# Performance work log

Measured on AMD Instinct MI355X. Metric: run time of the kernel, lower is better.

The kernel has to match this reference:

```python
import jax, jax.numpy as jnp
import numpy as np
from jax import lax

N = 8192

def _conv(x, w, b):
    # x: NCHW, w: OIHW, valid conv stride 1
    y = lax.conv_general_dilated(x, w, (1, 1), 'VALID',
                                 dimension_numbers=('NCHW', 'OIHW', 'NCHW'))
    return y + b[None, :, None, None]

def _maxpool2(x):
    return lax.reduce_window(x, -jnp.inf, lax.max, (1, 1, 2, 2), (1, 1, 2, 2), 'VALID')

def setup_inputs() -> dict:
    key = jax.random.key(0)
    ks = jax.random.split(key, 13)
    def rn(k, shape, scale):
        return jax.random.normal(k, shape, dtype=jnp.float32) * scale
    inp = {}
    inp['x'] = jax.random.normal(ks[0], (N, 3, 32, 32), dtype=jnp.float32)
    inp['W1'] = rn(ks[1], (6, 3, 5, 5), 0.1)
    inp['b1'] = rn(ks[2], (6,), 0.1)
    inp['W2'] = rn(ks[3], (16, 6, 5, 5), 0.08)
    inp['b2'] = rn(ks[4], (16,), 0.1)
    inp['Wf1'] = rn(ks[5], (120, 400), 0.05)
    inp['bf1'] = rn(ks[6], (120,), 0.05)
    inp['Wf2'] = rn(ks[7], (84, 120), 0.09)
    inp['bf2'] = rn(ks[8], (84,), 0.09)
    inp['Wg'] = rn(ks[9], (10, 84), 0.1)    # GATConv fc weight (no bias)
    inp['attn_l'] = rn(ks[10], (10,), 0.3)  # a_l (src)
    inp['attn_r'] = rn(ks[11], (10,), 0.3)  # a_r (dst)
    inp['bg'] = rn(ks[12], (10,), 0.1)      # GATConv output bias
    return inp

def reference(x, W1, b1, W2, b2, Wf1, bf1, Wf2, bf2, Wg, attn_l, attn_r, bg):
    # CNN feature extractor (LeNet style)
    h = _maxpool2(jax.nn.relu(_conv(x, W1, b1)))   # [N,6,14,14]
    h = _maxpool2(jax.nn.relu(_conv(h, W2, b2)))   # [N,16,5,5]
    h = h.reshape(-1, 16 * 5 * 5)                  # [N,400]
    h = jax.nn.relu(h @ Wf1.T + bf1)               # [N,120]
    h = jax.nn.relu(h @ Wf2.T + bf2)               # [N,84]
    # Single-head GAT over fully-connected graph (incl. self-loops):
    # equivalent dense formulation of DGL GATConv(84,10,1)
    z = h @ Wg.T                                    # [N,10]
    el = z @ attn_l                                 # src scores [N]
    er = z @ attn_r                                 # dst scores [N]
    # e[i,j]: edge src=j -> dst=i
    e = jax.nn.leaky_relu(er[:, None] + el[None, :], negative_slope=0.2)  # [N,N]
    alpha = jax.nn.softmax(e, axis=1)               # softmax over incoming edges
    out = alpha @ z + bg                            # [N,10]
    return out
```

## Files before the change

kernel.cpp:

```cpp
#include <hip/hip_runtime.h>
#include <hip/hip_bf16.h>

typedef _Float16 half8 __attribute__((ext_vector_type(8)));
typedef __attribute__((aligned(8))) half8 half8_a8;
typedef float floatx4 __attribute__((ext_vector_type(4)));

#define LOG2E 1.44269504088896340736f

__device__ __forceinline__ float pool4_dpp(float v) {
  int s1 = __builtin_amdgcn_update_dpp(0, __float_as_int(v), 0xB1, 0xF, 0xF, true);
  float v1 = fmaxf(v, __int_as_float(s1));
  int s2 = __builtin_amdgcn_update_dpp(0, __float_as_int(v1), 0x4E, 0xF, 0xF, true);
  return fmaxf(v1, __int_as_float(s2));
}

__global__ __launch_bounds__(256) void k_prep(const float* __restrict__ Wf1,
    const float* __restrict__ Wf2, const float* __restrict__ Wg,
    const float* __restrict__ W1, const float* __restrict__ W2,
    _Float16* __restrict__ w1f, _Float16* __restrict__ w2f,
    _Float16* __restrict__ wgf, _Float16* __restrict__ B1,
    _Float16* __restrict__ B2M) {
  const int i = blockIdx.x * 256 + threadIdx.x;
  if (i < 53248) {
    const int n = i / 416, k = i - n * 416;
    w1f[i] = (_Float16)((n < 120 && k < 400) ? Wf1[n * 400 + k] : 0.f);
  } else if (i < 65536) {
    const int j = i - 53248;
    const int n = j >> 7, k = j & 127;
    w2f[j] = (_Float16)((n < 84 && k < 120) ? Wf2[n * 120 + k] : 0.f);
  } else if (i < 67072) {
    const int g = i - 65536;
    const int n = g / 96, k = g - n * 96;
    wgf[g] = (_Float16)((n < 10 && k < 84) ? Wg[n * 84 + k] : 0.f);
  } else if (i < 73216) {
    const int g = i - 67072;
    const int n = g / 192, k = g - n * 192;
    const int co = n >> 2, cy = (n >> 1) & 1, cx = n & 1;
    const int pidx = k >> 3, j = k & 7;
    const int r = pidx >> 2, ci = pidx & 3;
    float v = 0.f;
    if (co < 6 && ci < 3) {
      const int ky = r - cy, kx = j - cx;
      if (ky >= 0 && ky < 5 && kx >= 0 && kx < 5)
        v = W1[((co * 3 + ci) * 5 + ky) * 5 + kx];
    }
    B1[g] = (_Float16)v;
  } else if (i < 77312) {
    const int g = i - 73216;
    const int n = g >> 8, k = g & 255;
    float v = 0.f;
    if (k < 240) {
      const int ci = k / 40, rem = k - ci * 40, r = rem >> 3, j = rem & 7;
      if (j < 5) v = W2[((n * 6 + ci) * 5 + r) * 5 + j];
    }
    B2M[g] = (_Float16)v;
  }
}

__global__ __launch_bounds__(256) void k_conv1(const float* __restrict__ x,
    const _Float16* __restrict__ B1, const float* __restrict__ b1,
    _Float16* __restrict__ h1) {
  __shared__ __align__(16) char sm[15552];
  const int t = threadIdx.x;
  const float4* x4 = (const float4*)(x + (size_t)blockIdx.x * 3072);
  for (int i = t; i < 768; i += 256) {
    const float4 v = x4[i];
    const int ci = i >> 8, rem2 = i & 255;
    const int y = rem2 >> 3, c = rem2 & 7;
    union { _Float16 h[2]; unsigned u; } p01, p23;
    p01.h[0] = (_Float16)v.x; p01.h[1] = (_Float16)v.y;
    p23.h[0] = (_Float16)v.z; p23.h[1] = (_Float16)v.w;
    char* row = sm + ci * 5184 + y * 80;
    *(uint2*)(row + 8 * c) = make_uint2(p01.u, p23.u);
    *(unsigned*)(row + 2596 + 8 * c) = p01.u;
    *(unsigned*)(row + 2600 + 8 * c) = p23.u;
  }
  if (t < 96) {
    const int ci = t >> 5, y = t & 31;
    *(unsigned*)(sm + ci * 5184 + 2596 + y * 80 + 64) = 0u;
  }
  __syncthreads();
  const int w4 = t >> 6, lane = t & 63;
  const int l16 = lane & 15, q = lane >> 4;
  const int px = l16;
  const int colOff = (px & 1) ? (2596 + 4 * px) : (4 * px);
  const char* base = sm + ((q == 3) ? 0 : q * 5184) + colOff;
  half8 bfr[2][6];
#pragma unroll
  for (int nt = 0; nt < 2; nt++)
#pragma unroll
    for (int kc = 0; kc < 6; kc++)
      bfr[nt][kc] =
          *(const half8*)(B1 + (size_t)(nt * 16 + l16) * 192 + kc * 32 + q * 8);
  const int co_n = l16 >> 2;
  const int co1 = 4 + co_n;
  const float bias0 = b1[co_n];
  const float bias1 = (co1 < 6) ? b1[co1] : 0.f;
  const int py0 = (7 * w4) >> 1;
  const int py1 = (7 * (w4 + 1)) >> 1;
  half8 a[6];
#pragma unroll
  for (int r = 0; r < 6; r++)
    a[r] = *(const half8_a8*)(base + (2 * py0 + r) * 80);
  const size_t ob = (size_t)blockIdx.x * 1176;
  const bool store_lane = (l16 & 3) == 0;
  for (int py = py0; py < py1; ++py) {
    floatx4 acc0, acc1;
#pragma unroll
    for (int r = 0; r < 4; r++) { acc0[r] = 0.f; acc1[r] = 0.f; }
#pragma unroll
    for (int kc = 0; kc < 6; kc++) {
      acc0 = __builtin_amdgcn_mfma_f32_16x16x32_f16(a[kc], bfr[0][kc], acc0, 0, 0, 0);
      acc1 = __builtin_amdgcn_mfma_f32_16x16x32_f16(a[kc], bfr[1][kc], acc1, 0, 0, 0);
    }
    if (py < py1 - 1) {
      a[0] = a[2]; a[1] = a[3]; a[2] = a[4]; a[3] = a[5];
      a[4] = *(const half8_a8*)(base + (2 * py + 6) * 80);
      a[5] = *(const half8_a8*)(base + (2 * py + 7) * 80);
    }
    float p0[4], p1[4];
#pragma unroll
    for (int r = 0; r < 4; r++) {
      p0[r] = fmaxf(pool4_dpp(acc0[r]) + bias0, 0.f);
      p1[r] = fmaxf(pool4_dpp(acc1[r]) + bias1, 0.f);
    }
    if (store_lane) {
      union { _Float16 h[2]; unsigned u; } s01, s23;
      s01.h[0] = (_Float16)p0[0]; s01.h[1] = (_Float16)p0[1];
      s23.h[0] = (_Float16)p0[2]; s23.h[1] = (_Float16)p0[3];
      _Float16* dst = h1 + ob + co_n * 196 + py * 14 + q * 4;
      *(unsigned*)dst = s01.u;
      if (q < 3) *(unsigned*)(dst + 2) = s23.u;
      if (co1 < 6) {
        union { _Float16 h[2]; unsigned u; } t01, t23;
        t01.h[0] = (_Float16)p1[0]; t01.h[1] = (_Float16)p1[1];
        t23.h[0] = (_Float16)p1[2]; t23.h[1] = (_Float16)p1[3];
        _Float16* dst1 = h1 + ob + co1 * 196 + py * 14 + q * 4;
        *(unsigned*)dst1 = t01.u;
        if (q < 3) *(unsigned*)(dst1 + 2) = t23.u;
      }
    }
  }
}

__global__ __launch_bounds__(256) void k_conv2(const _Float16* __restrict__ h1,
    const _Float16* __restrict__ B2M, const float* __restrict__ b2,
    _Float16* __restrict__ h2) {
  __shared__ __align__(16) char sm[22272];
  const int t = threadIdx.x;
  const int n0 = blockIdx.x * 2;
  if (t < 168) {
    const int img = t / 84, rem = t - img * 84;
    const int ci = rem / 14, y = rem - ci * 14;
    const unsigned* src =
        (const unsigned*)(h1 + (size_t)(n0 + img) * 1176 + ci * 196 + y * 14);
    unsigned u[10];
#pragma unroll
    for (int k = 0; k < 7; k++) u[k] = src[k];
    u[7] = 0u; u[8] = 0u; u[9] = 0u;
    char* base = sm + img * 11136 + ci * 1856 + y * 32;
#pragma unroll
    for (int ww = 0; ww < 8; ww++) {
      *(unsigned*)(base + 4 * ww) = u[ww];
      *(unsigned*)(base + 464 + 4 * ww) = (u[ww] >> 16) | (u[ww + 1] << 16);
      *(unsigned*)(base + 928 + 4 * ww) = u[ww + 1];
      *(unsigned*)(base + 1392 + 4 * ww) = (u[ww + 1] >> 16) | (u[ww + 2] << 16);
    }
  }
  if (t < 32) {
    const int im = t >> 4;
    h2[(size_t)(n0 + im) * 416 + 400 + (t & 15)] = (_Float16)0.f;
  }
  __syncthreads();
  const int w = t >> 6, lane = t & 63;
  const int l16 = lane & 15, q = lane >> 4;
  int C2[8];
#pragma unroll
  for (int kc = 0; kc < 8; kc++) {
    const int pidx = kc * 4 + q;
    C2[kc] = (pidx < 30) ? (pidx / 5) * 1856 + (pidx % 5) * 32 : 0;
  }
  half8 bfr[8];
#pragma unroll
  for (int kc = 0; kc < 8; kc++)
    bfr[kc] = *(const half8*)(B2M + (size_t)l16 * 256 + kc * 32 + q * 8);
  const float bias = b2[l16];
  for (int mt = w; mt < 13; mt += 4) {
    const int m = min(mt * 16 + l16, 199);
    const int pos = m >> 2, cy = (m >> 1) & 1, cx = m & 1;
    const int img = pos / 25, p = pos - img * 25;
    const int py = p / 5, px = p - py * 5;
    const int h = 2 * px + cx, s = h & 3;
    const char* base =
        sm + img * 11136 + s * 464 + (2 * py + cy) * 32 + (h - s) * 2;
    half8 a[8];
#pragma unroll
    for (int kc = 0; kc < 8; kc++) a[kc] = *(const half8_a8*)(base + C2[kc]);
    floatx4 acc;
#pragma unroll
    for (int r = 0; r < 4; r++) acc[r] = 0.f;
#pragma unroll
    for (int kc = 0; kc < 8; kc++)
      acc = __builtin_amdgcn_mfma_f32_16x16x32_f16(a[kc], bfr[kc], acc, 0, 0, 0);
    const float v = fmaxf(fmaxf(acc[0], acc[1]), fmaxf(acc[2], acc[3]));
    const int posL = mt * 4 + q;
    if (posL < 50) {
      const int im = posL / 25, pp = posL - im * 25;
      h2[(size_t)(n0 + im) * 416 + l16 * 25 + pp] =
          (_Float16)fmaxf(v + bias, 0.f);
    }
  }
}

__global__ __launch_bounds__(256) void k_mlp(
    const _Float16* __restrict__ h2, const _Float16* __restrict__ w1,
    const float* __restrict__ bf1, const _Float16* __restrict__ w2,
    const float* __restrict__ bf2, const _Float16* __restrict__ wg,
    const float* __restrict__ al, const float* __restrict__ ar,
    _Float16* __restrict__ zT, float* __restrict__ el, float* __restrict__ er) {
  __shared__ __align__(16) _Float16 h3s[32 * 136];
  __shared__ __align__(16) _Float16 h4s[32 * 104];
  __shared__ float zs[32 * 17];
  const int t = threadIdx.x;
  const int w = t >> 6, lane = t & 63;
  const int l16 = lane & 15, q = lane >> 4;
  const int row0 = blockIdx.x * 32;
  for (int i = t; i < 2176; i += 256) ((float*)h3s)[i] = 0.f;
  for (int i = t; i < 1664; i += 256) ((float*)h4s)[i] = 0.f;
  const int rt = w & 1, cg = w >> 1;
  const int am = row0 + rt * 16 + l16;
  floatx4 acc[4];
#pragma unroll
  for (int ct = 0; ct < 4; ct++)
#pragma unroll
    for (int r = 0; r < 4; r++) acc[ct][r] = 0.f;
  const half8* Ag = (const half8*)(h2 + (size_t)am * 416 + q * 8);
  for (int kc = 0; kc < 13; kc++) {
    half8 a = Ag[kc * 4];
#pragma unroll
    for (int ct = 0; ct < 4; ct++) {
      const int n = cg * 64 + ct * 16 + l16;
      half8 b = *(const half8*)(w1 + (size_t)n * 416 + kc * 32 + q * 8);
      acc[ct] = __builtin_amdgcn_mfma_f32_16x16x32_f16(a, b, acc[ct], 0, 0, 0);
    }
  }
  __syncthreads();
#pragma unroll
  for (int ct = 0; ct < 4; ct++) {
    const int n = cg * 64 + ct * 16 + l16;
    if (n < 120) {
      const float bias = bf1[n];
#pragma unroll
      for (int r = 0; r < 4; r++) {
        const int rr = rt * 16 + q * 4 + r;
        h3s[rr * 136 + n] = (_Float16)fmaxf(acc[ct][r] + bias, 0.f);
      }
    }
  }
  __syncthreads();
  const int cbase2 = (w >> 1) * 3;
  floatx4 acc2[3];
#pragma unroll
  for (int ct = 0; ct < 3; ct++)
#pragma unroll
    for (int r = 0; r < 4; r++) acc2[ct][r] = 0.f;
  const _Float16* A2 = h3s + (rt * 16 + l16) * 136 + q * 8;
  for (int kc = 0; kc < 4; kc++) {
    half8 a = *(const half8*)(A2 + kc * 32);
#pragma unroll
    for (int ct = 0; ct < 3; ct++) {
      const int n = (cbase2 + ct) * 16 + l16;
      half8 b = *(const half8*)(w2 + (size_t)n * 128 + kc * 32 + q * 8);
      acc2[ct] = __builtin_amdgcn_mfma_f32_16x16x32_f16(a, b, acc2[ct], 0, 0, 0);
    }
  }
  __syncthreads();
#pragma unroll
  for (int ct = 0; ct < 3; ct++) {
    const int n = (cbase2 + ct) * 16 + l16;
    if (n < 84) {
      const float bias = bf2[n];
#pragma unroll
      for (int r = 0; r < 4; r++) {
        const int rr = rt * 16 + q * 4 + r;
        h4s[rr * 104 + n] = (_Float16)fmaxf(acc2[ct][r] + bias, 0.f);
      }
    }
  }
  __syncthreads();
  if (w < 2) {
    floatx4 acc3;
#pragma unroll
    for (int r = 0; r < 4; r++) acc3[r] = 0.f;
    const _Float16* A3 = h4s + (w * 16 + l16) * 104 + q * 8;
    for (int kc = 0; kc < 3; kc++) {
      half8 a = *(const half8*)(A3 + kc * 32);
      half8 b = *(const half8*)(wg + (size_t)l16 * 96 + kc * 32 + q * 8);
      acc3 = __builtin_amdgcn_mfma_f32_16x16x32_f16(a, b, acc3, 0, 0, 0);
    }
#pragma unroll
    for (int r = 0; r < 4; r++) {
      const int rr = w * 16 + q * 4 + r;
      zs[rr * 17 + l16] = acc3[r];
    }
  }
  __syncthreads();
  if (t < 32) {
    float e1 = 0.f, e2 = 0.f;
#pragma unroll
    for (int d = 0; d < 10; d++) {
      const float zv = zs[t * 17 + d];
      e1 += zv * al[d];
      e2 += zv * ar[d];
    }
    el[row0 + t] = e1 * LOG2E;
    er[row0 + t] = e2 * LOG2E;
  }
  for (int idx = t; idx < 352; idx += 256) {
    const int d = idx >> 5, c = idx & 31;
    zT[(size_t)d * 8192 + row0 + c] =
        (d < 10) ? (_Float16)zs[c * 17 + d] : (_Float16)1.0f;
  }
}

__global__ __launch_bounds__(256) void k_elmax(const float* __restrict__ el,
                                               float* __restrict__ out) {
  __shared__ float red[4];
  const int t = threadIdx.x;
  float m = -1e30f;
  for (int i = t; i < 8192; i += 256) m = fmaxf(m, el[i]);
#pragma unroll
  for (int off = 32; off > 0; off >>= 1) m = fmaxf(m, __shfl_down(m, off, 64));
  if ((t & 63) == 0) red[t >> 6] = m;
  __syncthreads();
  if (t == 0) out[0] = fmaxf(fmaxf(red[0], red[1]), fmaxf(red[2], red[3]));
}

__global__ __launch_bounds__(256) void k_attn(const _Float16* __restrict__ zT,
    const float* __restrict__ el, const float* __restrict__ er,
    const float* __restrict__ elmax, float* __restrict__ part) {
  const int t = threadIdx.x;
  const int w = t >> 6, lane = t & 63;
  const int l16 = lane & 15, q = lane >> 4;
  const int itile = blockIdx.x * 64 + w * 16;
  const int jb = blockIdx.y * 1024;
  const float mx = elmax[0];
  const float eri = er[itile + l16];
  const float s0 = eri + mx;
  const float mi = fmaxf(s0, 0.2f * s0);
  floatx4 acc;
#pragma unroll
  for (int r = 0; r < 4; r++) acc[r] = 0.f;
  const float* elp = el + jb + q * 8;
  const _Float16* ztp = zT + (size_t)l16 * 8192 + jb + q * 8;
  for (int jc = 0; jc < 32; jc++) {
    const float4 e0 = *(const float4*)(elp + jc * 32);
    const float4 e1 = *(const float4*)(elp + jc * 32 + 4);
    float wf[8];
    const float ej[8] = {e0.x, e0.y, e0.z, e0.w, e1.x, e1.y, e1.z, e1.w};
#pragma unroll
    for (int u = 0; u < 8; u++) {
      const float s = eri + ej[u];
      const float lr = fmaxf(s, 0.2f * s);
      wf[u] = exp2f(lr - mi);
    }
    half8 a;
#pragma unroll
    for (int u = 0; u < 8; u++) a[u] = (_Float16)wf[u];
    const half8 b = *(const half8*)(ztp + jc * 32);
    acc = __builtin_amdgcn_mfma_f32_16x16x32_f16(a, b, acc, 0, 0, 0);
  }
  if (l16 < 11) {
    float* pp = part + (size_t)blockIdx.y * 98304 + (size_t)l16 * 8192 + itile + q * 4;
#pragma unroll
    for (int r = 0; r < 4; r++) pp[r] = acc[r];
  }
}

__global__ __launch_bounds__(256) void k_final(const float* __restrict__ part,
    const float* __restrict__ bg, float* __restrict__ out) {
  __shared__ float red[8][32][12];
  const int t = threadIdx.x;
  const int i0 = blockIdx.x * 32;
  const int il = t & 31, sg = t >> 5;
  const float* pp = part + (size_t)sg * 98304 + i0 + il;
#pragma unroll
  for (int d = 0; d < 11; d++) red[sg][il][d] = pp[d * 8192];
  __syncthreads();
  for (int t2 = t; t2 < 352; t2 += 256) {
    const int ii = t2 / 11, d = t2 - ii * 11;
    if (d < 10) {
      float num = 0.f, den = 0.f;
#pragma unroll
      for (int s = 0; s < 8; s++) {
        num += red[s][ii][d];
        den += red[s][ii][10];
      }
      out[(size_t)(i0 + ii) * 10 + d] = num / den + bg[d];
    }
  }
}

extern "C" void kernel_launch(void* const* d_in, const int* in_sizes, int n_in,
                              void* d_out, int out_size, void* d_ws, size_t ws_size,
                              hipStream_t stream) {
  const float* x   = (const float*)d_in[0];
  const float* W1  = (const float*)d_in[1];
  const float* b1  = (const float*)d_in[2];
  const float* W2  = (const float*)d_in[3];
  const float* b2  = (const float*)d_in[4];
  const float* Wf1 = (const float*)d_in[5];
  const float* bf1 = (const float*)d_in[6];
  const float* Wf2 = (const float*)d_in[7];
  const float* bf2 = (const float*)d_in[8];
  const float* Wg  = (const float*)d_in[9];
  const float* al  = (const float*)d_in[10];
  const float* ar  = (const float*)d_in[11];
  const float* bg  = (const float*)d_in[12];
  float* out = (float*)d_out;

  float* ws = (float*)d_ws;
  _Float16* h1f = (_Float16*)ws;
  float* p = ws + (size_t)8192 * 588;
  _Float16* h2f = (_Float16*)p;
  p += (size_t)8192 * 208;
  _Float16* zTf = (_Float16*)p; p += 65536;
  float* el  = p; p += 8192;
  float* er  = p; p += 8192;
  float* emx = p; p += 16;
  _Float16* w1f = (_Float16*)p; p += 26624;
  _Float16* w2f = (_Float16*)p; p += 6144;
  _Float16* wgf = (_Float16*)p; p += 768;
  _Float16* B1g = (_Float16*)p; p += 3072;
  _Float16* B2g = (_Float16*)p; p += 2048;
  float* part = ws;

  k_prep<<<302, 256, 0, stream>>>(Wf1, Wf2, Wg, W1, W2, w1f, w2f, wgf, B1g, B2g);
  k_conv1<<<8192, 256, 0, stream>>>(x, B1g, b1, h1f);
  k_conv2<<<4096, 256, 0, stream>>>(h1f, B2g, b2, h2f);
  k_mlp<<<256, 256, 0, stream>>>(h2f, w1f, bf1, w2f, bf2, wgf, al, ar, zTf, el, er);
  k_elmax<<<1, 256, 0, stream>>>(el, emx);
  dim3 ag(128, 8);
  k_attn<<<ag, 256, 0, stream>>>(zTf, el, er, emx, part);
  k_final<<<256, 256, 0, stream>>>(part, bg, out);
}
```

Before: 284.3 us.

## Fuse conv1 and conv2 into one kernel keeping pooled h1 in shared memory

Merges the two convolution kernels into a single kernel that processes two images per block: conv1+pool writes its fp16 output into LDS, then conv2 reads it from LDS after a barrier. This removes the global write and reread of the h1 intermediate (about 19 MB) and one kernel launch. It raises LDS use per block to about 35 KB, which may lower occupancy, and adds extra barriers. Each conv1 wave now handles 7 pooled rows of one image instead of splitting 14 rows across four waves.

```diff
diff --git a/kernel.cpp b/kernel.cpp
--- a/kernel.cpp
+++ b/kernel.cpp
@@ -57,103 +57,111 @@
   }
 }
 
-__global__ __launch_bounds__(256) void k_conv1(const float* __restrict__ x,
+__global__ __launch_bounds__(256) void k_convs(const float* __restrict__ x,
     const _Float16* __restrict__ B1, const float* __restrict__ b1,
-    _Float16* __restrict__ h1) {
-  __shared__ __align__(16) char sm[15552];
+    const _Float16* __restrict__ B2M, const float* __restrict__ b2,
+    _Float16* __restrict__ h2) {
+  __shared__ __align__(16) char sm[35808];
+  _Float16* h1L = (_Float16*)(sm + 31104);
   const int t = threadIdx.x;
-  const float4* x4 = (const float4*)(x + (size_t)blockIdx.x * 3072);
-  for (int i = t; i < 768; i += 256) {
+  const int n0 = blockIdx.x * 2;
+  const int w4 = t >> 6, lane = t & 63;
+  const int l16 = lane & 15, q = lane >> 4;
+
+  const float4* x4 = (const float4*)(x + (size_t)n0 * 3072);
+  for (int i = t; i < 1536; i += 256) {
     const float4 v = x4[i];
-    const int ci = i >> 8, rem2 = i & 255;
+    const int img = (i >= 768);
+    const int ii = i - img * 768;
+    const int ci = ii >> 8, rem2 = ii & 255;
     const int y = rem2 >> 3, c = rem2 & 7;
     union { _Float16 h[2]; unsigned u; } p01, p23;
     p01.h[0] = (_Float16)v.x; p01.h[1] = (_Float16)v.y;
     p23.h[0] = (_Float16)v.z; p23.h[1] = (_Float16)v.w;
-    char* row = sm + ci * 5184 + y * 80;
+    char* row = sm + img * 15552 + ci * 5184 + y * 80;
     *(uint2*)(row + 8 * c) = make_uint2(p01.u, p23.u);
     *(unsigned*)(row + 2596 + 8 * c) = p01.u;
     *(unsigned*)(row + 2600 + 8 * c) = p23.u;
   }
-  if (t < 96) {
-    const int ci = t >> 5, y = t & 31;
-    *(unsigned*)(sm + ci * 5184 + 2596 + y * 80 + 64) = 0u;
-  }
-  __syncthreads();
-  const int w4 = t >> 6, lane = t & 63;
-  const int l16 = lane & 15, q = lane >> 4;
-  const int px = l16;
-  const int colOff = (px & 1) ? (2596 + 4 * px) : (4 * px);
-  const char* base = sm + ((q == 3) ? 0 : q * 5184) + colOff;
-  half8 bfr[2][6];
-#pragma unroll
-  for (int nt = 0; nt < 2; nt++)
-#pragma unroll
-    for (int kc = 0; kc < 6; kc++)
-      bfr[nt][kc] =
-          *(const half8*)(B1 + (size_t)(nt * 16 + l16) * 192 + kc * 32 + q * 8);
-  const int co_n = l16 >> 2;
-  const int co1 = 4 + co_n;
-  const float bias0 = b1[co_n];
-  const float bias1 = (co1 < 6) ? b1[co1] : 0.f;
-  const int py0 = (7 * w4) >> 1;
-  const int py1 = (7 * (w4 + 1)) >> 1;
-  half8 a[6];
-#pragma unroll
-  for (int r = 0; r < 6; r++)
-    a[r] = *(const half8_a8*)(base + (2 * py0 + r) * 80);
-  const size_t ob = (size_t)blockIdx.x * 1176;
-  const bool store_lane = (l16 & 3) == 0;
-  for (int py = py0; py < py1; ++py) {
-    floatx4 acc0, acc1;
-#pragma unroll
-    for (int r = 0; r < 4; r++) { acc0[r] = 0.f; acc1[r] = 0.f; }
-#pragma unroll
-    for (int kc = 0; kc < 6; kc++) {
-      acc0 = __builtin_amdgcn_mfma_f32_16x16x32_f16(a[kc], bfr[0][kc], acc0, 0, 0, 0);
-      acc1 = __builtin_amdgcn_mfma_f32_16x16x32_f16(a[kc], bfr[1][kc], acc1, 0, 0, 0);
-    }
-    if (py < py1 - 1) {
-      a[0] = a[2]; a[1] = a[3]; a[2] = a[4]; a[3] = a[5];
-      a[4] = *(const half8_a8*)(base + (2 * py + 6) * 80);
-      a[5] = *(const half8_a8*)(base + (2 * py + 7) * 80);
-    }
-    float p0[4], p1[4];
-#pragma unroll
-    for (int r = 0; r < 4; r++) {
-      p0[r] = fmaxf(pool4_dpp(acc0[r]) + bias0, 0.f);
-      p1[r] = fmaxf(pool4_dpp(acc1[r]) + bias1, 0.f);
-    }
-    if (store_lane) {
-      union { _Float16 h[2]; unsigned u; } s01, s23;
-      s01.h[0] = (_Float16)p0[0]; s01.h[1] = (_Float16)p0[1];
-      s23.h[0] = (_Float16)p0[2]; s23.h[1] = (_Float16)p0[3];
-      _Float16* dst = h1 + ob + co_n * 196 + py * 14 + q * 4;
-      *(unsigned*)dst = s01.u;
-      if (q < 3) *(unsigned*)(dst + 2) = s23.u;
-      if (co1 < 6) {
-        union { _Float16 h[2]; unsigned u; } t01, t23;
-        t01.h[0] = (_Float16)p1[0]; t01.h[1] = (_Float16)p1[1];
-        t23.h[0] = (_Float16)p1[2]; t23.h[1] = (_Float16)p1[3];
-        _Float16* dst1 = h1 + ob + co1 * 196 + py * 14 + q * 4;
-        *(unsigned*)dst1 = t01.u;
-        if (q < 3) *(unsigned*)(dst1 + 2) = t23.u;
-      }
-    }
-  }
-}
-
-__global__ __launch_bounds__(256) void k_conv2(const _Float16* __restrict__ h1,
-    const _Float16* __restrict__ B2M, const float* __restrict__ b2,
-    _Float16* __restrict__ h2) {
-  __shared__ __align__(16) char sm[22272];
-  const int t = threadIdx.x;
-  const int n0 = blockIdx.x * 2;
+  if (t < 192) {
+    const int img = t / 96, tt = t - img * 96;
+    const int ci = tt >> 5, y = tt & 31;
+    *(unsigned*)(sm + img * 15552 + ci * 5184 + 2596 + y * 80 + 64) = 0u;
+  }
+  if (t < 32) {
+    const int im = t >> 4;
+    h2[(size_t)(n0 + im) * 416 + 400 + (t & 15)] = (_Float16)0.f;
+  }
+  __syncthreads();
+
+  {
+    const int img = w4 >> 1, wl = w4 & 1;
+    const int px = l16;
+    const int colOff = (px & 1) ? (2596 + 4 * px) : (4 * px);
+    const char* base = sm + img * 15552 + ((q == 3) ? 0 : q * 5184) + colOff;
+    half8 bfr[2][6];
+#pragma unroll
+    for (int nt = 0; nt < 2; nt++)
+#pragma unroll
+      for (int kc = 0; kc < 6; kc++)
+        bfr[nt][kc] =
+            *(const half8*)(B1 + (size_t)(nt * 16 + l16) * 192 + kc * 32 + q * 8);
+    const int co_n = l16 >> 2;
+    const int co1 = 4 + co_n;
+    const float bias0 = b1[co_n];
+    const float bias1 = (co1 < 6) ? b1[co1] : 0.f;
+    const int py0 = wl * 7;
+    const int py1 = py0 + 7;
+    half8 a[6];
+#pragma unroll
+    for (int r = 0; r < 6; r++)
+      a[r] = *(const half8_a8*)(base + (2 * py0 + r) * 80);
+    _Float16* dstb = h1L + img * 1176;
+    const bool store_lane = (l16 & 3) == 0;
+    for (int py = py0; py < py1; ++py) {
+      floatx4 acc0, acc1;
+#pragma unroll
+      for (int r = 0; r < 4; r++) { acc0[r] = 0.f; acc1[r] = 0.f; }
+#pragma unroll
+      for (int kc = 0; kc < 6; kc++) {
+        acc0 = __builtin_amdgcn_mfma_f32_16x16x32_f16(a[kc], bfr[0][kc], acc0, 0, 0, 0);
+        acc1 = __builtin_amdgcn_mfma_f32_16x16x32_f16(a[kc], bfr[1][kc], acc1, 0, 0, 0);
+      }
+      if (py < py1 - 1) {
+        a[0] = a[2]; a[1] = a[3]; a[2] = a[4]; a[3] = a[5];
+        a[4] = *(const half8_a8*)(base + (2 * py + 6) * 80);
+        a[5] = *(const half8_a8*)(base + (2 * py + 7) * 80);
+      }
+      float p0[4], p1[4];
+#pragma unroll
+      for (int r = 0; r < 4; r++) {
+        p0[r] = fmaxf(pool4_dpp(acc0[r]) + bias0, 0.f);
+        p1[r] = fmaxf(pool4_dpp(acc1[r]) + bias1, 0.f);
+      }
+      if (store_lane) {
+        union { _Float16 h[2]; unsigned u; } s01, s23;
+        s01.h[0] = (_Float16)p0[0]; s01.h[1] = (_Float16)p0[1];
+        s23.h[0] = (_Float16)p0[2]; s23.h[1] = (_Float16)p0[3];
+        _Float16* dst = dstb + co_n * 196 + py * 14 + q * 4;
+        *(unsigned*)dst = s01.u;
+        if (q < 3) *(unsigned*)(dst + 2) = s23.u;
+        if (co1 < 6) {
+          union { _Float16 h[2]; unsigned u; } t01, t23;
+          t01.h[0] = (_Float16)p1[0]; t01.h[1] = (_Float16)p1[1];
+          t23.h[0] = (_Float16)p1[2]; t23.h[1] = (_Float16)p1[3];
+          _Float16* dst1 = dstb + co1 * 196 + py * 14 + q * 4;
+          *(unsigned*)dst1 = t01.u;
+          if (q < 3) *(unsigned*)(dst1 + 2) = t23.u;
+        }
+      }
+    }
+  }
+  __syncthreads();
+
   if (t < 168) {
     const int img = t / 84, rem = t - img * 84;
     const int ci = rem / 14, y = rem - ci * 14;
-    const unsigned* src =
-        (const unsigned*)(h1 + (size_t)(n0 + img) * 1176 + ci * 196 + y * 14);
+    const unsigned* src = (const unsigned*)(h1L + img * 1176 + ci * 196 + y * 14);
     unsigned u[10];
 #pragma unroll
     for (int k = 0; k < 7; k++) u[k] = src[k];
@@ -167,47 +175,44 @@
       *(unsigned*)(base + 1392 + 4 * ww) = (u[ww + 1] >> 16) | (u[ww + 2] << 16);
     }
   }
-  if (t < 32) {
-    const int im = t >> 4;
-    h2[(size_t)(n0 + im) * 416 + 400 + (t & 15)] = (_Float16)0.f;
-  }
-  __syncthreads();
-  const int w = t >> 6, lane = t & 63;
-  const int l16 = lane & 15, q = lane >> 4;
-  int C2[8];
-#pragma unroll
-  for (int kc = 0; kc < 8; kc++) {
-    const int pidx = kc * 4 + q;
-    C2[kc] = (pidx < 30) ? (pidx / 5) * 1856 + (pidx % 5) * 32 : 0;
-  }
-  half8 bfr[8];
-#pragma unroll
-  for (int kc = 0; kc < 8; kc++)
-    bfr[kc] = *(const half8*)(B2M + (size_t)l16 * 256 + kc * 32 + q * 8);
-  const float bias = b2[l16];
-  for (int mt = w; mt < 13; mt += 4) {
-    const int m = min(mt * 16 + l16, 199);
-    const int pos = m >> 2, cy = (m >> 1) & 1, cx = m & 1;
-    const int img = pos / 25, p = pos - img * 25;
-    const int py = p / 5, px = p - py * 5;
-    const int h = 2 * px + cx, s = h & 3;
-    const char* base =
-        sm + img * 11136 + s * 464 + (2 * py + cy) * 32 + (h - s) * 2;
-    half8 a[8];
-#pragma unroll
-    for (int kc = 0; kc < 8; kc++) a[kc] = *(const half8_a8*)(base + C2[kc]);
-    floatx4 acc;
-#pragma unroll
-    for (int r = 0; r < 4; r++) acc[r] = 0.f;
+  __syncthreads();
+
+  {
+    int C2[8];
+#pragma unroll
+    for (int kc = 0; kc < 8; kc++) {
+      const int pidx = kc * 4 + q;
+      C2[kc] = (pidx < 30) ? (pidx / 5) * 1856 + (pidx % 5) * 32 : 0;
+    }
+    half8 bfr[8];
 #pragma unroll
     for (int kc = 0; kc < 8; kc++)
-      acc = __builtin_amdgcn_mfma_f32_16x16x32_f16(a[kc], bfr[kc], acc, 0, 0, 0);
-    const float v = fmaxf(fmaxf(acc[0], acc[1]), fmaxf(acc[2], acc[3]));
-    const int posL = mt * 4 + q;
-    if (posL < 50) {
-      const int im = posL / 25, pp = posL - im * 25;
-      h2[(size_t)(n0 + im) * 416 + l16 * 25 + pp] =
-          (_Float16)fmaxf(v + bias, 0.f);
+      bfr[kc] = *(const half8*)(B2M + (size_t)l16 * 256 + kc * 32 + q * 8);
+    const float bias = b2[l16];
+    for (int mt = w4; mt < 13; mt += 4) {
+      const int m = min(mt * 16 + l16, 199);
+      const int pos = m >> 2, cy = (m >> 1) & 1, cx = m & 1;
+      const int img = pos / 25, p = pos - img * 25;
+      const int py = p / 5, px = p - py * 5;
+      const int h = 2 * px + cx, s = h & 3;
+      const char* base =
+          sm + img * 11136 + s * 464 + (2 * py + cy) * 32 + (h - s) * 2;
+      half8 a[8];
+#pragma unroll
+      for (int kc = 0; kc < 8; kc++) a[kc] = *(const half8_a8*)(base + C2[kc]);
+      floatx4 acc;
+#pragma unroll
+      for (int r = 0; r < 4; r++) acc[r] = 0.f;
+#pragma unroll
+      for (int kc = 0; kc < 8; kc++)
+        acc = __builtin_amdgcn_mfma_f32_16x16x32_f16(a[kc], bfr[kc], acc, 0, 0, 0);
+      const float v = fmaxf(fmaxf(acc[0], acc[1]), fmaxf(acc[2], acc[3]));
+      const int posL = mt * 4 + q;
+      if (posL < 50) {
+        const int im = posL / 25, pp = posL - im * 25;
+        h2[(size_t)(n0 + im) * 416 + l16 * 25 + pp] =
+            (_Float16)fmaxf(v + bias, 0.f);
+      }
     }
   }
 }
@@ -420,7 +425,6 @@
   float* out = (float*)d_out;
 
   float* ws = (float*)d_ws;
-  _Float16* h1f = (_Float16*)ws;
   float* p = ws + (size_t)8192 * 588;
   _Float16* h2f = (_Float16*)p;
   p += (size_t)8192 * 208;
@@ -436,8 +440,7 @@
   float* part = ws;
 
   k_prep<<<302, 256, 0, stream>>>(Wf1, Wf2, Wg, W1, W2, w1f, w2f, wgf, B1g, B2g);
-  k_conv1<<<8192, 256, 0, stream>>>(x, B1g, b1, h1f);
-  k_conv2<<<4096, 256, 0, stream>>>(h1f, B2g, b2, h2f);
+  k_convs<<<4096, 256, 0, stream>>>(x, B1g, b1, B2g, b2, h2f);
   k_mlp<<<256, 256, 0, stream>>>(h2f, w1f, bf1, w2f, bf2, wgf, al, ar, zTf, el, er);
   k_elmax<<<1, 256, 0, stream>>>(el, emx);
   dim3 ag(128, 8);
```

Measured after the change: 257.5 us. 9.4% less time.
